# Kernel optimization log

Hardware: AMD Instinct MI355X
Metric: run time of the kernel (lower is better)

Reference implementation:

```python
import jax, jax.numpy as jnp
import numpy as np

E = 8          # num_workers == number of experts (one expert per data-parallel rank)
EPS = 1e-5     # LayerNorm eps


def setup_inputs() -> dict:
    key = jax.random.key(0)
    ks = jax.random.split(key, 6)
    d, f = 1024, 4096
    B, S = 2, 1024
    x = jax.random.normal(ks[0], (B, S, d), dtype=jnp.float32)
    # expert centroids: orthogonal init with gain 0.1, shape [E, d]
    c = jax.random.normal(ks[1], (d, E), dtype=jnp.float32)
    q, _ = jnp.linalg.qr(c)                       # [d, E], orthonormal columns
    centroids = (0.1 * q.T).astype(jnp.float32)   # [E, d]
    # per-expert BaseSublayer params (each worker owns its own expert_network)
    w1 = jax.random.normal(ks[2], (E, d, f), dtype=jnp.float32) / np.sqrt(d).astype(np.float32)
    b1 = jnp.zeros((E, f), dtype=jnp.float32)
    # note: original zero-inits ff2.weight; we use small random so output is non-trivial
    w2 = jax.random.normal(ks[3], (E, f, d), dtype=jnp.float32) * 0.02
    b2 = jnp.zeros((E, d), dtype=jnp.float32)
    gamma = jnp.ones((E, d), dtype=jnp.float32)
    beta = jnp.zeros((E, d), dtype=jnp.float32)
    return dict(x=x, centroids=centroids, w1=w1, b1=b1, w2=w2, b2=b2,
                gamma=gamma, beta=beta)


def reference(x, centroids, w1, b1, w2, b2, gamma, beta):
    B, S, d = x.shape
    feats = x.reshape(-1, d)                         # [T, d] tokens
    # token->expert affinities (no_grad in original; argmax is non-diff anyway)
    aff = feats @ centroids.T                        # [T, E]
    eid = jnp.argmax(aff, axis=1)                    # greedy_assignment, k=1
    # shared (affine-free) layernorm statistics, computed once
    mu = jnp.mean(feats, axis=-1, keepdims=True)
    var = jnp.var(feats, axis=-1, keepdims=True)
    xhat = (feats - mu) * jax.lax.rsqrt(var + EPS)   # [T, d]
    out = jnp.zeros_like(feats)
    for e in range(E):                               # small fixed expert loop
        mask = (eid == e).astype(feats.dtype)[:, None]
        h = xhat * gamma[e] + beta[e]
        y = feats + jax.nn.relu(h @ w1[e] + b1[e]) @ w2[e] + b2[e]  # BaseSublayer
        alpha = jax.nn.sigmoid(feats @ centroids[e])[:, None]       # gate vs own centroid
        out = out + mask * (alpha * y + (1.0 - alpha) * feats)
    return out.reshape(B, S, d)
```

## Files before the change

### kernel.cpp

```cpp
#include <hip/hip_runtime.h>
#include <hip/hip_bf16.h>

#define T_TOK 2048
#define D_MODEL 1024
#define F_FF 4096
#define N_EXP 8
#define BM 64
#define MAXMT (T_TOK / BM + N_EXP)
#define LNEPS 1e-5f

typedef __bf16 bf16x8 __attribute__((ext_vector_type(8)));
typedef float f32x4 __attribute__((ext_vector_type(4)));

__global__ __launch_bounds__(64) void assign_kernel(
    const float* __restrict__ x, const float* __restrict__ cent,
    int* __restrict__ eid, int* __restrict__ rank, float* __restrict__ alpha,
    float* __restrict__ mu, float* __restrict__ rstd, int* __restrict__ cnt)
{
    const int t = blockIdx.x;
    const int lane = threadIdx.x;
    const float* xr = x + (size_t)t * D_MODEL;

    float s = 0.f, sq = 0.f;
    float dot[N_EXP];
#pragma unroll
    for (int e = 0; e < N_EXP; e++) dot[e] = 0.f;

#pragma unroll
    for (int i0 = 0; i0 < D_MODEL; i0 += 256) {
        const int i = i0 + lane * 4;
        float4 v = *(const float4*)&xr[i];
        s  += v.x + v.y + v.z + v.w;
        sq += v.x * v.x + v.y * v.y + v.z * v.z + v.w * v.w;
#pragma unroll
        for (int e = 0; e < N_EXP; e++) {
            float4 c = *(const float4*)&cent[(size_t)e * D_MODEL + i];
            dot[e] += v.x * c.x + v.y * c.y + v.z * c.z + v.w * c.w;
        }
    }
#pragma unroll
    for (int off = 32; off > 0; off >>= 1) {
        s  += __shfl_down(s, off);
        sq += __shfl_down(sq, off);
#pragma unroll
        for (int e = 0; e < N_EXP; e++) dot[e] += __shfl_down(dot[e], off);
    }
    if (lane == 0) {
        float m = s * (1.f / D_MODEL);
        float var = sq * (1.f / D_MODEL) - m * m;
        int be = 0; float bv = dot[0];
#pragma unroll
        for (int e = 1; e < N_EXP; e++) { if (dot[e] > bv) { bv = dot[e]; be = e; } }
        eid[t] = be;
        alpha[t] = 1.f / (1.f + __expf(-bv));
        mu[t] = m;
        rstd[t] = rsqrtf(var + LNEPS);
        rank[t] = atomicAdd(&cnt[be], 1);
    }
}

__global__ void plan_kernel(const int* __restrict__ cnt, int* __restrict__ segBase,
                            int* __restrict__ tileE, int* __restrict__ tileRow,
                            int* __restrict__ numTiles)
{
    if (threadIdx.x == 0 && blockIdx.x == 0) {
        int off = 0, nt = 0;
        for (int e = 0; e < N_EXP; e++) {
            segBase[e] = off;
            int tiles = (cnt[e] + BM - 1) / BM;
            for (int i = 0; i < tiles; i++) { tileE[nt] = e; tileRow[nt] = off + i * BM; nt++; }
            off += tiles * BM;
        }
        *numTiles = nt;
    }
}

__global__ __launch_bounds__(64) void scatter_kernel(
    const float* __restrict__ x, const float* __restrict__ gamma, const float* __restrict__ beta,
    const int* __restrict__ eid, const int* __restrict__ rank, const float* __restrict__ alpha,
    const int* __restrict__ segBase, const float* __restrict__ mu, const float* __restrict__ rstd,
    __bf16* __restrict__ Hin, int* __restrict__ tokSorted, float* __restrict__ alphaSorted)
{
    const int t = blockIdx.x;
    const int lane = threadIdx.x;
    const int e = eid[t];
    const int pos = segBase[e] + rank[t];
    if (lane == 0) { tokSorted[pos] = t; alphaSorted[pos] = alpha[t]; }
    const float m = mu[t], r = rstd[t];
    const float* xr = x + (size_t)t * D_MODEL;
    const float* g = gamma + (size_t)e * D_MODEL;
    const float* b = beta + (size_t)e * D_MODEL;
    __bf16* hr = Hin + (size_t)pos * D_MODEL;
#pragma unroll
    for (int i0 = 0; i0 < D_MODEL; i0 += 256) {
        const int i = i0 + lane * 4;
        float4 v = *(const float4*)&xr[i];
        float4 gv = *(const float4*)&g[i];
        float4 bv = *(const float4*)&b[i];
        __bf16 o[4];
        o[0] = (__bf16)((v.x - m) * r * gv.x + bv.x);
        o[1] = (__bf16)((v.y - m) * r * gv.y + bv.y);
        o[2] = (__bf16)((v.z - m) * r * gv.z + bv.z);
        o[3] = (__bf16)((v.w - m) * r * gv.w + bv.w);
        *(uint2*)&hr[i] = *(const uint2*)o;
    }
}

template<int KD, int ND, bool FINAL>
__global__ __launch_bounds__(256) void gemm_kernel(
    const __bf16* __restrict__ A, const float* __restrict__ Wall,
    const float* __restrict__ bias,
    __bf16* __restrict__ Gout,
    float* __restrict__ out, const float* __restrict__ x,
    const int* __restrict__ tokSorted, const float* __restrict__ alphaSorted,
    const int* __restrict__ tileE, const int* __restrict__ tileRow,
    const int* __restrict__ numTiles)
{
    const int mt = blockIdx.y;
    if (mt >= *numTiles) return;
    const int e = tileE[mt];
    const int row0 = tileRow[mt];
    const int n0 = blockIdx.x * 64;
    const float* W = Wall + (size_t)e * KD * ND;
    const int tid = threadIdx.x;

    __shared__ __align__(16) __bf16 As[64 * 72];
    __shared__ __align__(16) __bf16 Bs[64 * 72];

    f32x4 acc[2][2] = {};

    const int lane = tid & 63;
    const int wv = tid >> 6;
    const int mbase = (wv >> 1) * 32, nbase = (wv & 1) * 32;
    const int kl = (lane >> 4) * 8, rl = lane & 15;

    const int ar = tid >> 2, ac = (tid & 3) * 8;
    const int bk = tid >> 4, bn = (tid & 15) * 4;

    for (int k0 = 0; k0 < KD; k0 += 64) {
        const __bf16* asrc = A + (size_t)(row0 + ar) * KD + k0 + ac;
        *(uint4*)&As[ar * 72 + ac]      = *(const uint4*)asrc;
        *(uint4*)&As[ar * 72 + ac + 32] = *(const uint4*)(asrc + 32);
#pragma unroll
        for (int j = 0; j < 4; j++) {
            int k = bk + j * 16;
            float4 w4 = *(const float4*)&W[(size_t)(k0 + k) * ND + n0 + bn];
            Bs[(bn + 0) * 72 + k] = (__bf16)w4.x;
            Bs[(bn + 1) * 72 + k] = (__bf16)w4.y;
            Bs[(bn + 2) * 72 + k] = (__bf16)w4.z;
            Bs[(bn + 3) * 72 + k] = (__bf16)w4.w;
        }
        __syncthreads();
#pragma unroll
        for (int kk = 0; kk < 64; kk += 32) {
            bf16x8 a0 = *(const bf16x8*)&As[(mbase + rl) * 72 + kk + kl];
            bf16x8 a1 = *(const bf16x8*)&As[(mbase + 16 + rl) * 72 + kk + kl];
            bf16x8 b0 = *(const bf16x8*)&Bs[(nbase + rl) * 72 + kk + kl];
            bf16x8 b1 = *(const bf16x8*)&Bs[(nbase + 16 + rl) * 72 + kk + kl];
            acc[0][0] = __builtin_amdgcn_mfma_f32_16x16x32_bf16(a0, b0, acc[0][0], 0, 0, 0);
            acc[0][1] = __builtin_amdgcn_mfma_f32_16x16x32_bf16(a0, b1, acc[0][1], 0, 0, 0);
            acc[1][0] = __builtin_amdgcn_mfma_f32_16x16x32_bf16(a1, b0, acc[1][0], 0, 0, 0);
            acc[1][1] = __builtin_amdgcn_mfma_f32_16x16x32_bf16(a1, b1, acc[1][1], 0, 0, 0);
        }
        __syncthreads();
    }

#pragma unroll
    for (int mi = 0; mi < 2; mi++)
#pragma unroll
        for (int ni = 0; ni < 2; ni++) {
            const int gr0 = row0 + mbase + mi * 16 + (lane >> 4) * 4;
            const int gc = n0 + nbase + ni * 16 + rl;
            const float bv = bias[(size_t)e * ND + gc];
            if constexpr (!FINAL) {
#pragma unroll
                for (int j = 0; j < 4; j++) {
                    float v = acc[mi][ni][j] + bv;
                    Gout[(size_t)(gr0 + j) * ND + gc] = (__bf16)(v > 0.f ? v : 0.f);
                }
            } else {
#pragma unroll
                for (int j = 0; j < 4; j++) {
                    const int gr = gr0 + j;
                    const unsigned tok = (unsigned)tokSorted[gr];
                    if (tok < (unsigned)T_TOK) {
                        const size_t oi = (size_t)tok * ND + gc;
                        out[oi] = x[oi] + alphaSorted[gr] * (acc[mi][ni][j] + bv);
                    }
                }
            }
        }
}

extern "C" void kernel_launch(void* const* d_in, const int* in_sizes, int n_in,
                              void* d_out, int out_size, void* d_ws, size_t ws_size,
                              hipStream_t stream)
{
    const float* x    = (const float*)d_in[0];
    const float* cent = (const float*)d_in[1];
    const float* w1   = (const float*)d_in[2];
    const float* b1   = (const float*)d_in[3];
    const float* w2   = (const float*)d_in[4];
    const float* b2   = (const float*)d_in[5];
    const float* gamma= (const float*)d_in[6];
    const float* beta = (const float*)d_in[7];
    float* out = (float*)d_out;

    char* ws = (char*)d_ws;
    int*   cnt        = (int*)(ws + 0);
    int*   numTiles   = (int*)(ws + 32);
    int*   segBase    = (int*)(ws + 64);
    int*   tileE      = (int*)(ws + 128);
    int*   tileRow    = (int*)(ws + 384);
    int*   eid        = (int*)(ws + 1024);
    int*   rank       = (int*)(ws + 9216);
    float* alpha      = (float*)(ws + 17408);
    float* mu         = (float*)(ws + 25600);
    float* rstd       = (float*)(ws + 33792);
    int*   tokSorted  = (int*)(ws + 41984);
    float* alphaSorted= (float*)(ws + 52224);
    __bf16* Hin       = (__bf16*)(ws + 65536);
    __bf16* G         = (__bf16*)(ws + 65536 + 2560 * 1024 * 2);

    hipMemsetAsync(cnt, 0, 32, stream);

    assign_kernel<<<T_TOK, 64, 0, stream>>>(x, cent, eid, rank, alpha, mu, rstd, cnt);
    plan_kernel<<<1, 64, 0, stream>>>(cnt, segBase, tileE, tileRow, numTiles);
    scatter_kernel<<<T_TOK, 64, 0, stream>>>(x, gamma, beta, eid, rank, alpha,
                                             segBase, mu, rstd, Hin, tokSorted, alphaSorted);
    gemm_kernel<D_MODEL, F_FF, false><<<dim3(F_FF / 64, MAXMT), 256, 0, stream>>>(
        Hin, w1, b1, G, nullptr, nullptr, nullptr, nullptr, tileE, tileRow, numTiles);
    gemm_kernel<F_FF, D_MODEL, true><<<dim3(D_MODEL / 64, MAXMT), 256, 0, stream>>>(
        G, w2, b2, nullptr, out, x, tokSorted, alphaSorted, tileE, tileRow, numTiles);
}
```

Baseline: 472.4 us.

## Pre-transpose weights to bf16, use 128x128 LDS-direct GEMM tiles, split-K second GEMM

Adds a per-call kernel that converts and transposes each expert's fp32 weights to bf16 K-major layout, so the GEMM loads B with direct global-to-LDS 16-byte copies into an XOR-swizzled shared buffer. GEMM tiles grow from 64x64 to 128x128 with a 4x4 MFMA grid per wave. The second GEMM is split four ways along K, writing bf16 partials that a new reduce kernel sums and combines with bias, gate and residual. The costs added are extra traffic for the weight transposes on every call, storage and traffic for the partial buffers, and bf16 rounding of the partial sums.

```diff
diff --git a/kernel.cpp b/kernel.cpp
--- a/kernel.cpp
+++ b/kernel.cpp
@@ -5,12 +5,20 @@
 #define D_MODEL 1024
 #define F_FF 4096
 #define N_EXP 8
-#define BM 64
+#define BM 128
 #define MAXMT (T_TOK / BM + N_EXP)
+#define MROWS 3072
 #define LNEPS 1e-5f
+#define WSTRIDE 4194304
 
 typedef __bf16 bf16x8 __attribute__((ext_vector_type(8)));
 typedef float f32x4 __attribute__((ext_vector_type(4)));
+
+__device__ __forceinline__ void gload16(const void* g, void* l) {
+    __builtin_amdgcn_global_load_lds(
+        (const __attribute__((address_space(1))) unsigned int*)g,
+        (__attribute__((address_space(3))) unsigned int*)l, 16, 0, 0);
+}
 
 __global__ __launch_bounds__(64) void assign_kernel(
     const float* __restrict__ x, const float* __restrict__ cent,
@@ -106,13 +114,47 @@
     }
 }
 
-template<int KD, int ND, bool FINAL>
+template<int K, int N>
+__global__ __launch_bounds__(256) void wtrans_kernel(
+    const float* __restrict__ W, __bf16* __restrict__ Wt)
+{
+    constexpr int TPE = (K / 64) * (N / 64);
+    const int b = blockIdx.x;
+    const int e = b / TPE;
+    const int t = b % TPE;
+    const int kt = t / (N / 64);
+    const int nt = t % (N / 64);
+    const float* in = W + (size_t)e * K * N + (size_t)kt * 64 * N + nt * 64;
+    __bf16* outp = Wt + (size_t)e * K * N + (size_t)nt * 64 * K + kt * 64;
+    __shared__ float lds[64 * 67];
+    const int tid = threadIdx.x;
+#pragma unroll
+    for (int i = 0; i < 4; ++i) {
+        int idx = tid + i * 256;
+        int r = idx >> 4, c4 = (idx & 15) * 4;
+        float4 v = *(const float4*)&in[(size_t)r * N + c4];
+        lds[r * 67 + c4 + 0] = v.x;
+        lds[r * 67 + c4 + 1] = v.y;
+        lds[r * 67 + c4 + 2] = v.z;
+        lds[r * 67 + c4 + 3] = v.w;
+    }
+    __syncthreads();
+#pragma unroll
+    for (int i = 0; i < 2; ++i) {
+        int idx = tid + i * 256;
+        int orow = idx >> 3, g = idx & 7;
+        __bf16 o[8];
+#pragma unroll
+        for (int j = 0; j < 8; ++j)
+            o[j] = (__bf16)lds[(g * 8 + j) * 67 + orow];
+        *(uint4*)&outp[(size_t)orow * K + g * 8] = *(const uint4*)o;
+    }
+}
+
+template<int LDA, int LDB, int LDOUT, bool FINAL>
 __global__ __launch_bounds__(256) void gemm_kernel(
-    const __bf16* __restrict__ A, const float* __restrict__ Wall,
-    const float* __restrict__ bias,
-    __bf16* __restrict__ Gout,
-    float* __restrict__ out, const float* __restrict__ x,
-    const int* __restrict__ tokSorted, const float* __restrict__ alphaSorted,
+    const __bf16* __restrict__ A, const __bf16* __restrict__ Wt,
+    const float* __restrict__ bias, __bf16* __restrict__ Out,
     const int* __restrict__ tileE, const int* __restrict__ tileRow,
     const int* __restrict__ numTiles)
 {
@@ -120,76 +162,107 @@
     if (mt >= *numTiles) return;
     const int e = tileE[mt];
     const int row0 = tileRow[mt];
-    const int n0 = blockIdx.x * 64;
-    const float* W = Wall + (size_t)e * KD * ND;
+    const int n0 = blockIdx.x * 128;
+    const int z = blockIdx.z;
+    const int k0base = z * 1024;
+
     const int tid = threadIdx.x;
-
-    __shared__ __align__(16) __bf16 As[64 * 72];
-    __shared__ __align__(16) __bf16 Bs[64 * 72];
-
-    f32x4 acc[2][2] = {};
-
-    const int lane = tid & 63;
-    const int wv = tid >> 6;
-    const int mbase = (wv >> 1) * 32, nbase = (wv & 1) * 32;
-    const int kl = (lane >> 4) * 8, rl = lane & 15;
-
-    const int ar = tid >> 2, ac = (tid & 3) * 8;
-    const int bk = tid >> 4, bn = (tid & 15) * 4;
-
-    for (int k0 = 0; k0 < KD; k0 += 64) {
-        const __bf16* asrc = A + (size_t)(row0 + ar) * KD + k0 + ac;
-        *(uint4*)&As[ar * 72 + ac]      = *(const uint4*)asrc;
-        *(uint4*)&As[ar * 72 + ac + 32] = *(const uint4*)(asrc + 32);
-#pragma unroll
-        for (int j = 0; j < 4; j++) {
-            int k = bk + j * 16;
-            float4 w4 = *(const float4*)&W[(size_t)(k0 + k) * ND + n0 + bn];
-            Bs[(bn + 0) * 72 + k] = (__bf16)w4.x;
-            Bs[(bn + 1) * 72 + k] = (__bf16)w4.y;
-            Bs[(bn + 2) * 72 + k] = (__bf16)w4.z;
-            Bs[(bn + 3) * 72 + k] = (__bf16)w4.w;
+    const int l = tid & 63, wv = tid >> 6;
+    const int wr = wv >> 1, wc = wv & 1;
+    const int rl = l & 15, kh = l >> 4;
+
+    __shared__ __align__(16) __bf16 As[128 * 64];
+    __shared__ __align__(16) __bf16 Bs[128 * 64];
+
+    const __bf16* Ab = A + (size_t)row0 * LDA;
+    const __bf16* Bb = Wt + (size_t)e * WSTRIDE + (size_t)n0 * LDB;
+
+    f32x4 acc[4][4] = {};
+
+    for (int it = 0; it < 16; ++it) {
+        const int k0 = k0base + it * 64;
+#pragma unroll
+        for (int c = 0; c < 4; ++c) {
+            const int chunk = wv * 4 + c;
+            const int g = chunk * 64 + l;
+            const int row = g >> 3;
+            const int cs = (g & 7) ^ (row & 7);
+            gload16(Ab + (size_t)row * LDA + k0 + cs * 8, (char*)As + chunk * 1024);
+            gload16(Bb + (size_t)row * LDB + k0 + cs * 8, (char*)Bs + chunk * 1024);
         }
         __syncthreads();
 #pragma unroll
         for (int kk = 0; kk < 64; kk += 32) {
-            bf16x8 a0 = *(const bf16x8*)&As[(mbase + rl) * 72 + kk + kl];
-            bf16x8 a1 = *(const bf16x8*)&As[(mbase + 16 + rl) * 72 + kk + kl];
-            bf16x8 b0 = *(const bf16x8*)&Bs[(nbase + rl) * 72 + kk + kl];
-            bf16x8 b1 = *(const bf16x8*)&Bs[(nbase + 16 + rl) * 72 + kk + kl];
-            acc[0][0] = __builtin_amdgcn_mfma_f32_16x16x32_bf16(a0, b0, acc[0][0], 0, 0, 0);
-            acc[0][1] = __builtin_amdgcn_mfma_f32_16x16x32_bf16(a0, b1, acc[0][1], 0, 0, 0);
-            acc[1][0] = __builtin_amdgcn_mfma_f32_16x16x32_bf16(a1, b0, acc[1][0], 0, 0, 0);
-            acc[1][1] = __builtin_amdgcn_mfma_f32_16x16x32_bf16(a1, b1, acc[1][1], 0, 0, 0);
+            bf16x8 a[4], b[4];
+            const int kg = (kk >> 3) + kh;
+#pragma unroll
+            for (int i = 0; i < 4; ++i) {
+                const int ar = wr * 64 + i * 16 + rl;
+                a[i] = *(const bf16x8*)((const char*)As + ar * 128 + ((kg ^ (ar & 7)) * 16));
+                const int br = wc * 64 + i * 16 + rl;
+                b[i] = *(const bf16x8*)((const char*)Bs + br * 128 + ((kg ^ (br & 7)) * 16));
+            }
+#pragma unroll
+            for (int mi = 0; mi < 4; ++mi)
+#pragma unroll
+                for (int ni = 0; ni < 4; ++ni)
+                    acc[mi][ni] = __builtin_amdgcn_mfma_f32_16x16x32_bf16(a[mi], b[ni], acc[mi][ni], 0, 0, 0);
         }
         __syncthreads();
     }
 
 #pragma unroll
-    for (int mi = 0; mi < 2; mi++)
-#pragma unroll
-        for (int ni = 0; ni < 2; ni++) {
-            const int gr0 = row0 + mbase + mi * 16 + (lane >> 4) * 4;
-            const int gc = n0 + nbase + ni * 16 + rl;
-            const float bv = bias[(size_t)e * ND + gc];
+    for (int mi = 0; mi < 4; ++mi)
+#pragma unroll
+        for (int ni = 0; ni < 4; ++ni) {
+            const int gr0 = row0 + wr * 64 + mi * 16 + kh * 4;
+            const int gc = n0 + wc * 64 + ni * 16 + rl;
             if constexpr (!FINAL) {
-#pragma unroll
-                for (int j = 0; j < 4; j++) {
+                const float bv = bias[(size_t)e * F_FF + gc];
+#pragma unroll
+                for (int j = 0; j < 4; ++j) {
                     float v = acc[mi][ni][j] + bv;
-                    Gout[(size_t)(gr0 + j) * ND + gc] = (__bf16)(v > 0.f ? v : 0.f);
+                    Out[(size_t)(gr0 + j) * LDOUT + gc] = (__bf16)(v > 0.f ? v : 0.f);
                 }
             } else {
-#pragma unroll
-                for (int j = 0; j < 4; j++) {
-                    const int gr = gr0 + j;
-                    const unsigned tok = (unsigned)tokSorted[gr];
-                    if (tok < (unsigned)T_TOK) {
-                        const size_t oi = (size_t)tok * ND + gc;
-                        out[oi] = x[oi] + alphaSorted[gr] * (acc[mi][ni][j] + bv);
-                    }
-                }
+                __bf16* outp = Out + (size_t)z * MROWS * D_MODEL;
+#pragma unroll
+                for (int j = 0; j < 4; ++j)
+                    outp[(size_t)(gr0 + j) * LDOUT + gc] = (__bf16)acc[mi][ni][j];
             }
         }
+}
+
+__global__ __launch_bounds__(256) void reduce_kernel(
+    const __bf16* __restrict__ P, const float* __restrict__ x,
+    const float* __restrict__ b2, const int* __restrict__ tokSorted,
+    const float* __restrict__ alphaSorted, const int* __restrict__ eid,
+    float* __restrict__ out)
+{
+    const int r = blockIdx.x;
+    const unsigned tok = (unsigned)tokSorted[r];
+    if (tok >= (unsigned)T_TOK) return;
+    const int e = eid[tok];
+    const float a = alphaSorted[r];
+    const int c = threadIdx.x * 4;
+    float s0 = 0.f, s1 = 0.f, s2 = 0.f, s3 = 0.f;
+#pragma unroll
+    for (int zz = 0; zz < 4; ++zz) {
+        const __bf16* p = P + ((size_t)zz * MROWS + r) * D_MODEL + c;
+        ushort4 v = *(const ushort4*)p;
+        s0 += __uint_as_float((unsigned)v.x << 16);
+        s1 += __uint_as_float((unsigned)v.y << 16);
+        s2 += __uint_as_float((unsigned)v.z << 16);
+        s3 += __uint_as_float((unsigned)v.w << 16);
+    }
+    float4 b = *(const float4*)&b2[(size_t)e * D_MODEL + c];
+    float4 xv = *(const float4*)&x[(size_t)tok * D_MODEL + c];
+    float4 o;
+    o.x = xv.x + a * (s0 + b.x);
+    o.y = xv.y + a * (s1 + b.y);
+    o.z = xv.z + a * (s2 + b.z);
+    o.w = xv.w + a * (s3 + b.w);
+    *(float4*)&out[(size_t)tok * D_MODEL + c] = o;
 }
 
 extern "C" void kernel_launch(void* const* d_in, const int* in_sizes, int n_in,
@@ -208,28 +281,34 @@
 
     char* ws = (char*)d_ws;
     int*   cnt        = (int*)(ws + 0);
-    int*   numTiles   = (int*)(ws + 32);
-    int*   segBase    = (int*)(ws + 64);
-    int*   tileE      = (int*)(ws + 128);
-    int*   tileRow    = (int*)(ws + 384);
+    int*   numTiles   = (int*)(ws + 64);
+    int*   segBase    = (int*)(ws + 128);
+    int*   tileE      = (int*)(ws + 256);
+    int*   tileRow    = (int*)(ws + 512);
     int*   eid        = (int*)(ws + 1024);
     int*   rank       = (int*)(ws + 9216);
     float* alpha      = (float*)(ws + 17408);
     float* mu         = (float*)(ws + 25600);
     float* rstd       = (float*)(ws + 33792);
     int*   tokSorted  = (int*)(ws + 41984);
-    float* alphaSorted= (float*)(ws + 52224);
-    __bf16* Hin       = (__bf16*)(ws + 65536);
-    __bf16* G         = (__bf16*)(ws + 65536 + 2560 * 1024 * 2);
-
-    hipMemsetAsync(cnt, 0, 32, stream);
+    float* alphaSorted= (float*)(ws + 54272);
+    __bf16* Hin = (__bf16*)(ws + 131072);
+    __bf16* G   = (__bf16*)(ws + 131072 + (size_t)MROWS*D_MODEL*2);
+    __bf16* Wt  = (__bf16*)(ws + 131072 + (size_t)MROWS*(D_MODEL+F_FF)*2);
+    __bf16* P   = (__bf16*)(ws + 131072 + (size_t)MROWS*(D_MODEL+F_FF)*2
+                                        + (size_t)N_EXP*WSTRIDE*2);
+
+    hipMemsetAsync(cnt, 0, 64, stream);
 
     assign_kernel<<<T_TOK, 64, 0, stream>>>(x, cent, eid, rank, alpha, mu, rstd, cnt);
     plan_kernel<<<1, 64, 0, stream>>>(cnt, segBase, tileE, tileRow, numTiles);
+    wtrans_kernel<D_MODEL, F_FF><<<8192, 256, 0, stream>>>(w1, Wt);
     scatter_kernel<<<T_TOK, 64, 0, stream>>>(x, gamma, beta, eid, rank, alpha,
                                              segBase, mu, rstd, Hin, tokSorted, alphaSorted);
-    gemm_kernel<D_MODEL, F_FF, false><<<dim3(F_FF / 64, MAXMT), 256, 0, stream>>>(
-        Hin, w1, b1, G, nullptr, nullptr, nullptr, nullptr, tileE, tileRow, numTiles);
-    gemm_kernel<F_FF, D_MODEL, true><<<dim3(D_MODEL / 64, MAXMT), 256, 0, stream>>>(
-        G, w2, b2, nullptr, out, x, tokSorted, alphaSorted, tileE, tileRow, numTiles);
-}
+    gemm_kernel<D_MODEL, D_MODEL, F_FF, false><<<dim3(F_FF / 128, MAXMT, 1), 256, 0, stream>>>(
+        Hin, Wt, b1, G, tileE, tileRow, numTiles);
+    wtrans_kernel<F_FF, D_MODEL><<<8192, 256, 0, stream>>>(w2, Wt);
+    gemm_kernel<F_FF, F_FF, D_MODEL, true><<<dim3(D_MODEL / 128, MAXMT, 4), 256, 0, stream>>>(
+        G, Wt, nullptr, P, tileE, tileRow, numTiles);
+    reduce_kernel<<<MROWS, 256, 0, stream>>>(P, x, b2, tokSorted, alphaSorted, eid, out);
+}
```

New measurement: 432.0 us. 1.09x faster.
